# Performance work log

Hardware: AMD Instinct MI355X
Metric: run time of the kernel (lower is better)

The kernel has to match this reference:

```python
import jax, jax.numpy as jnp
import numpy as np

K_SIZE = 12      # patch kernel/stride (non-overlapping)
H, W_IMG = 60, 108
PH, PW = H // K_SIZE, W_IMG // K_SIZE
L = PH * PW
N_LAYERS = 133
EPS = 1e-12


def _unfold(x):
    # x: [B, C, 60, 108] -> [B, C*12*12, 45], matching torch.nn.Unfold ordering
    B, C = x.shape[0], x.shape[1]
    x = x.reshape(B, C, PH, K_SIZE, PW, K_SIZE)          # (b,c,ph,ki,pw,kj)
    x = x.transpose(0, 1, 3, 5, 2, 4)                    # (b,c,ki,kj,ph,pw)
    return x.reshape(B, C * K_SIZE * K_SIZE, L)


def _fold(y, C=3):
    # y: [B, C*144, 45] -> [B, C, 60, 108] (non-overlapping, so fold = inverse reshape)
    B = y.shape[0]
    y = y.reshape(B, C, K_SIZE, K_SIZE, PH, PW)          # (b,c,ki,kj,ph,pw)
    y = y.transpose(0, 1, 4, 2, 5, 3)                    # (b,c,ph,ki,pw,kj)
    return y.reshape(B, C, H, W_IMG)


def setup_inputs() -> dict:
    key = jax.random.key(0)
    k1, k2, k3 = jax.random.split(key, 3)
    I = jax.random.normal(k1, (4, 3, H, W_IMG), dtype=jnp.float32)
    S = jax.random.uniform(k2, (4, H, W_IMG, N_LAYERS), dtype=jnp.float32)
    M = jax.random.uniform(k3, (4, 1, H, W_IMG), dtype=jnp.float32)
    return {"I": I, "S": S, "M": M}


def reference(I, S, M):
    bt = I.shape[0]
    Iu = I[..., None]                  # [bt,3,60,108,1]
    Se = S[:, None]                    # [bt,1,60,108,N]
    Me = M[..., None]                  # [bt,1,60,108,1]
    U = Iu * Se * Me                   # [bt,3,60,108,N]
    Kt = Iu * Se * (1.0 - Me)
    # permute(0,4,1,2,3).reshape(bt*N, 3, 60, 108)
    U = U.transpose(0, 4, 1, 2, 3).reshape(bt * N_LAYERS, 3, H, W_IMG)
    Kt = Kt.transpose(0, 4, 1, 2, 3).reshape(bt * N_LAYERS, 3, H, W_IMG)
    Ku = _unfold(Kt)                   # [B, 432, 45]
    Uu = _unfold(U)                    # [B, 432, 45]
    # affinity: bmm(U^T, K) -> [B, 45, 45]
    Wm = jnp.einsum('bcp,bcq->bpq', Uu, Ku)
    # F.normalize(p=1, dim=-1): divide by max(L1 norm, eps)
    l1 = jnp.maximum(jnp.sum(jnp.abs(Wm), axis=-1, keepdims=True), EPS)
    Wm = Wm / l1
    # weighted sum: WK[b,c,i] = sum_j W[b,i,j] * K[b,c,j]  (same math as the
    # original broadcast multiply+sum, expressed as a batched matmul)
    WK = jnp.einsum('bij,bcj->bci', Wm, Ku)              # [B, 432, 45]
    out = _fold(WK)                                       # [B, 3, 60, 108]
    out = out.reshape(bt, N_LAYERS, 3, H, W_IMG).sum(axis=1)
    return I * (1.0 - M) + out * M
```

## Files before the change

### kernel.cpp

```cpp
#include <hip/hip_runtime.h>

#define NL 133
#define HT 60
#define WD 108
#define PIX (HT*WD)
#define CT 432
#define L45 45
#define STR 440
#define BTC 4
#define NB (BTC*NL)
#define EPIX (3*PIX)

typedef _Float16 f16;
typedef _Float16 h4v __attribute__((ext_vector_type(4)));
typedef _Float16 h8v __attribute__((ext_vector_type(8)));
typedef float f32x4 __attribute__((ext_vector_type(4)));

__device__ __forceinline__ f32x4 mfma_k32(h8v a, h8v b, f32x4 c){
  return __builtin_amdgcn_mfma_f32_16x16x32_f16(a, b, c, 0, 0, 0);
}
__device__ __forceinline__ f32x4 mfma_k16(h4v a, h4v b, f32x4 c){
  return __builtin_amdgcn_mfma_f32_16x16x16f16(a, b, c, 0, 0, 0);
}

__global__ __launch_bounds__(256) void ktrans(const float* __restrict__ S,
                                              f16* __restrict__ St){
  __shared__ float tile[64][135];
  int blk = blockIdx.x;
  int bt = blk / 102, t = blk % 102;
  int pix0 = t * 64;
  int tid = threadIdx.x;
  for (int r = tid; r < 64*NL; r += 256){
    int p = r / NL, nn = r % NL;
    int pix = pix0 + p;
    if (pix < PIX) tile[p][nn] = S[((size_t)bt*PIX + pix)*NL + nn];
  }
  __syncthreads();
  for (int w = tid; w < 64*NL; w += 256){
    int nn = w / 64, p = w % 64;
    int pix = pix0 + p;
    if (pix < PIX) St[((size_t)(bt*NL + nn))*PIX + pix] = (f16)tile[p][nn];
  }
}

template<bool USE_SCR, bool USE_ST>
__global__ __launch_bounds__(256) void kmain(const float* __restrict__ I,
                                             const float* __restrict__ S,
                                             const float* __restrict__ M,
                                             const f16* __restrict__ St,
                                             f16* __restrict__ scr,
                                             float* __restrict__ outAcc){
  __shared__ f16 lds[(L45 + 48)*STR];
  f16* bufU = lds;
  f16* bufK = lds + L45*STR;

  int b  = blockIdx.x;
  int bt = b / NL, n = b % NL;
  int tid = threadIdx.x;
  const float* Ib = I + (size_t)bt*EPIX;
  const float* Mb = M + (size_t)bt*PIX;

  for (int z = tid; z < 3*STR; z += 256) bufK[L45*STR + z] = (f16)0.f;

  for (int c = tid; c < CT; c += 256){
    int ch = c / 144, kr = c % 144;
    int ky = kr / 12, kx = kr % 12;
    const float* Ich = Ib + ch*PIX;
    int p = 0;
    #pragma unroll
    for (int py = 0; py < 5; ++py){
      int row = (py*12 + ky)*WD;
      #pragma unroll
      for (int px = 0; px < 9; ++px, ++p){
        int x = px*12 + kx;
        float sv;
        if (USE_ST) sv = (float)St[(size_t)b*PIX + row + x];
        else        sv = S[((size_t)bt*PIX + row + x)*NL + n];
        float iv = Ich[row + x];
        float mv = Mb[row + x];
        float v = iv * sv;
        float u = v * mv;
        bufU[p*STR + c] = (f16)u;
        bufK[p*STR + c] = (f16)(v - u);
      }
    }
  }
  __syncthreads();

  int wid  = tid >> 6;
  int lane = tid & 63;
  int lrow = lane & 15, lgrp = lane >> 4;

  f32x4 acc0 = {0.f,0.f,0.f,0.f}, acc1 = acc0, acc2 = acc0;
  int t0 = wid;
  int t1 = wid + 4;
  int t2 = (wid + 8 < 9) ? wid + 8 : 8;
  int ti0 = t0/3, tj0 = t0%3;
  int ti1 = t1/3, tj1 = t1%3;
  int ti2 = t2/3, tj2 = t2%3;

  const f16* uA0 = &bufU[(ti0*16 + lrow)*STR];
  const f16* uA1 = &bufU[(ti1*16 + lrow)*STR];
  const f16* uA2 = &bufU[(ti2*16 + lrow)*STR];
  const f16* kB0 = &bufK[(tj0*16 + lrow)*STR];
  const f16* kB1 = &bufK[(tj1*16 + lrow)*STR];
  const f16* kB2 = &bufK[(tj2*16 + lrow)*STR];

  for (int ks = 0; ks < 13; ++ks){
    int c0 = ks*32 + lgrp*8;
    h8v a0 = *(const h8v*)&uA0[c0];
    h8v a1 = *(const h8v*)&uA1[c0];
    h8v a2 = *(const h8v*)&uA2[c0];
    h8v b0 = *(const h8v*)&kB0[c0];
    h8v b1 = *(const h8v*)&kB1[c0];
    h8v b2 = *(const h8v*)&kB2[c0];
    acc0 = mfma_k32(a0, b0, acc0);
    acc1 = mfma_k32(a1, b1, acc1);
    acc2 = mfma_k32(a2, b2, acc2);
  }
  {
    int c0 = 416 + lgrp*4;
    h4v a0 = *(const h4v*)&uA0[c0];
    h4v a1 = *(const h4v*)&uA1[c0];
    h4v a2 = *(const h4v*)&uA2[c0];
    h4v b0 = *(const h4v*)&kB0[c0];
    h4v b1 = *(const h4v*)&kB1[c0];
    h4v b2 = *(const h4v*)&kB2[c0];
    acc0 = mfma_k16(a0, b0, acc0);
    acc1 = mfma_k16(a1, b1, acc1);
    acc2 = mfma_k16(a2, b2, acc2);
  }
  __syncthreads();

  float* Wm32 = (float*)lds;
  f16*   Wm16 = (f16*)((char*)lds + 48*49*4);
  {
    #pragma unroll
    for (int r = 0; r < 4; ++r){
      Wm32[(ti0*16 + lgrp*4 + r)*49 + tj0*16 + lrow] = acc0[r];
      Wm32[(ti1*16 + lgrp*4 + r)*49 + tj1*16 + lrow] = acc1[r];
      Wm32[(ti2*16 + lgrp*4 + r)*49 + tj2*16 + lrow] = acc2[r];
    }
  }
  __syncthreads();

  if (tid < L45){
    float rs = 0.f;
    for (int q = 0; q < L45; ++q) rs += fabsf(Wm32[tid*49 + q]);
    float inv = 1.0f / fmaxf(rs, 1e-12f);
    for (int j = 0; j < 48; ++j)
      Wm16[tid*48 + j] = (j < L45) ? (f16)(Wm32[tid*49 + j]*inv) : (f16)0.f;
  }
  __syncthreads();

  h8v aw0 = *(const h8v*)&Wm16[( 0 + lrow)*48 + lgrp*8];
  h8v aw1 = *(const h8v*)&Wm16[(16 + lrow)*48 + lgrp*8];
  h8v aw2 = *(const h8v*)&Wm16[(32 + lrow)*48 + lgrp*8];
  h4v at0 = *(const h4v*)&Wm16[( 0 + lrow)*48 + 32 + lgrp*4];
  h4v at1 = *(const h4v*)&Wm16[(16 + lrow)*48 + 32 + lgrp*4];
  h4v at2 = *(const h4v*)&Wm16[(32 + lrow)*48 + 32 + lgrp*4];

  for (int cb = wid; cb < 27; cb += 4){
    int cbase = cb*16 + lrow;
    h8v bK; h4v bT;
    #pragma unroll
    for (int r = 0; r < 8; ++r) bK[r] = bufK[(lgrp*8 + r)*STR + cbase];
    #pragma unroll
    for (int r = 0; r < 4; ++r) bT[r] = bufK[(32 + lgrp*4 + r)*STR + cbase];

    int ch  = cb / 9;
    int kr  = (cb % 9)*16 + lrow;
    int ky  = kr / 12, kx = kr - ky*12;
    int pixc = ch*PIX + ky*WD + kx;

    f32x4 d0 = {0.f,0.f,0.f,0.f}, d1 = d0, d2 = d0;
    d0 = mfma_k32(aw0, bK, d0);  d0 = mfma_k16(at0, bT, d0);
    d1 = mfma_k32(aw1, bK, d1);  d1 = mfma_k16(at1, bT, d1);
    d2 = mfma_k32(aw2, bK, d2);  d2 = mfma_k16(at2, bT, d2);

    #pragma unroll
    for (int r = 0; r < 4; ++r){
      { int i = 0 + lgrp*4 + r;
        int iy = i/9, ix = i - iy*9;
        int pix = pixc + (iy*12)*WD + ix*12;
        if (USE_SCR) scr[(size_t)b*EPIX + pix] = (f16)d0[r];
        else atomicAdd(&outAcc[(size_t)bt*EPIX + pix], (float)d0[r]); }
      { int i = 16 + lgrp*4 + r;
        int iy = i/9, ix = i - iy*9;
        int pix = pixc + (iy*12)*WD + ix*12;
        if (USE_SCR) scr[(size_t)b*EPIX + pix] = (f16)d1[r];
        else atomicAdd(&outAcc[(size_t)bt*EPIX + pix], (float)d1[r]); }
      { int i = 32 + lgrp*4 + r;
        if (i < L45){
          int iy = i/9, ix = i - iy*9;
          int pix = pixc + (iy*12)*WD + ix*12;
          if (USE_SCR) scr[(size_t)b*EPIX + pix] = (f16)d2[r];
          else atomicAdd(&outAcc[(size_t)bt*EPIX + pix], (float)d2[r]); } }
    }
  }
}

__global__ __launch_bounds__(256) void kreduce(const float* __restrict__ I,
                                               const float* __restrict__ M,
                                               const f16* __restrict__ scr,
                                               float* __restrict__ out){
  int g = blockIdx.x*256 + threadIdx.x;
  if (g >= BTC*EPIX/4) return;
  int e4 = g*4;
  int bt = e4 / EPIX, e = e4 % EPIX;
  const f16* p = scr + (size_t)bt*NL*EPIX + e;
  float a0=0.f, a1=0.f, a2=0.f, a3=0.f;
  for (int nn = 0; nn < NL; ++nn){
    h4v v = *(const h4v*)&p[(size_t)nn*EPIX];
    a0 += (float)v[0]; a1 += (float)v[1]; a2 += (float)v[2]; a3 += (float)v[3];
  }
  int pixb = e % PIX;
  const float* Mb = M + (size_t)bt*PIX;
  float4 iv = *(const float4*)&I[e4];
  float m0 = Mb[pixb], m1 = Mb[pixb+1], m2 = Mb[pixb+2], m3 = Mb[pixb+3];
  float4 o;
  o.x = iv.x*(1.f-m0) + a0*m0;
  o.y = iv.y*(1.f-m1) + a1*m1;
  o.z = iv.z*(1.f-m2) + a2*m2;
  o.w = iv.w*(1.f-m3) + a3*m3;
  *(float4*)&out[e4] = o;
}

__global__ __launch_bounds__(256) void kfinal(const float* __restrict__ I,
                                              const float* __restrict__ M,
                                              float* __restrict__ out){
  int g = blockIdx.x*256 + threadIdx.x;
  if (g >= BTC*EPIX) return;
  int bt = g / EPIX, e = g % EPIX;
  float a = out[g];
  float m = M[bt*PIX + (e % PIX)];
  out[g] = I[g]*(1.f - m) + a*m;
}

extern "C" void kernel_launch(void* const* d_in, const int* in_sizes, int n_in,
                              void* d_out, int out_size, void* d_ws, size_t ws_size,
                              hipStream_t stream){
  const float* I = (const float*)d_in[0];
  const float* S = (const float*)d_in[1];
  const float* M = (const float*)d_in[2];
  float* out = (float*)d_out;

  const size_t needScr = (size_t)NB*EPIX*sizeof(f16);
  const size_t needSt  = (size_t)NB*PIX*sizeof(f16);

  bool useScr = ws_size >= needScr;
  bool useSt;
  f16* scr = (f16*)d_ws;
  f16* St;
  if (useScr){
    useSt = ws_size >= needScr + needSt;
    St = (f16*)((char*)d_ws + needScr);
  } else {
    useSt = ws_size >= needSt;
    St = (f16*)d_ws;
  }

  if (useSt) ktrans<<<BTC*102, 256, 0, stream>>>(S, St);

  if (useScr){
    if (useSt) kmain<true ,true ><<<NB, 256, 0, stream>>>(I, S, M, St, scr, out);
    else       kmain<true ,false><<<NB, 256, 0, stream>>>(I, S, M, St, scr, out);
    kreduce<<<(BTC*EPIX/4 + 255)/256, 256, 0, stream>>>(I, M, scr, out);
  } else {
    (void)hipMemsetAsync(out, 0, (size_t)BTC*EPIX*sizeof(float), stream);
    if (useSt) kmain<false,true ><<<NB, 256, 0, stream>>>(I, S, M, St, scr, out);
    else       kmain<false,false><<<NB, 256, 0, stream>>>(I, S, M, St, scr, out);
    kfinal<<<(BTC*EPIX + 255)/256, 256, 0, stream>>>(I, M, out);
  }
}
```

Measured before the change: 117.2 us.

## Pre-unfold S and I*M into patch layout, vectorize LDS fill, split reduce

The prep kernel now writes S in the unfolded patch-major order and also precomputes the unfolded I*M and I*(1-M) tensors in fp16. The main kernel's LDS staging becomes 8-wide vector loads and fp16 multiplies, replacing scattered strided fp32 gathers. The reduce kernel splits the 133-layer sum across 8 lanes and combines them with xor shuffles to add parallelism. The products are now formed in fp16 rather than fp32 before conversion, which costs some precision, and the new workspace layout requires the prep buffers to always fit.

```diff
diff --git a/kernel.cpp b/kernel.cpp
--- a/kernel.cpp
+++ b/kernel.cpp
@@ -23,31 +23,56 @@
   return __builtin_amdgcn_mfma_f32_16x16x16f16(a, b, c, 0, 0, 0);
 }
 
-__global__ __launch_bounds__(256) void ktrans(const float* __restrict__ S,
-                                              f16* __restrict__ St){
+__global__ __launch_bounds__(256) void kprep(const float* __restrict__ S,
+                                             const float* __restrict__ I,
+                                             const float* __restrict__ M,
+                                             f16* __restrict__ Su,
+                                             f16* __restrict__ IMu,
+                                             f16* __restrict__ IKu){
   __shared__ float tile[64][135];
   int blk = blockIdx.x;
-  int bt = blk / 102, t = blk % 102;
-  int pix0 = t * 64;
   int tid = threadIdx.x;
-  for (int r = tid; r < 64*NL; r += 256){
-    int p = r / NL, nn = r % NL;
-    int pix = pix0 + p;
-    if (pix < PIX) tile[p][nn] = S[((size_t)bt*PIX + pix)*NL + nn];
-  }
-  __syncthreads();
-  for (int w = tid; w < 64*NL; w += 256){
-    int nn = w / 64, p = w % 64;
-    int pix = pix0 + p;
-    if (pix < PIX) St[((size_t)(bt*NL + nn))*PIX + pix] = (f16)tile[p][nn];
-  }
-}
-
-template<bool USE_SCR, bool USE_ST>
-__global__ __launch_bounds__(256) void kmain(const float* __restrict__ I,
-                                             const float* __restrict__ S,
-                                             const float* __restrict__ M,
-                                             const f16* __restrict__ St,
+  if (blk < BTC*102){
+    int bt = blk / 102, t = blk % 102;
+    int pix0 = t * 64;
+    for (int r = tid; r < 64*NL; r += 256){
+      int p = r / NL, nn = r % NL;
+      int pix = pix0 + p;
+      if (pix < PIX) tile[p][nn] = S[((size_t)bt*PIX + pix)*NL + nn];
+    }
+    __syncthreads();
+    for (int w = tid; w < 64*NL; w += 256){
+      int nn = w / 64, pp = w % 64;
+      int pix = pix0 + pp;
+      if (pix < PIX){
+        int y = pix / WD, x = pix % WD;
+        int py = y/12, ky = y%12, px = x/12, kx = x%12;
+        int pa = py*9 + px, kr = ky*12 + kx;
+        Su[(size_t)(bt*NL + nn)*PIX + pa*144 + kr] = (f16)tile[pp][nn];
+      }
+    }
+  } else {
+    int b2 = blk - BTC*102;
+    int bt = b2 / L45, pa = b2 % L45;
+    int py = pa/9, px = pa%9;
+    const float* Ib = I + (size_t)bt*EPIX;
+    const float* Mb = M + (size_t)bt*PIX;
+    for (int c = tid; c < CT; c += 256){
+      int ch = c/144, kr = c%144;
+      int ky = kr/12, kx = kr%12;
+      int pix = (py*12 + ky)*WD + px*12 + kx;
+      float iv = Ib[ch*PIX + pix];
+      float mv = Mb[pix];
+      IMu[((size_t)bt*L45 + pa)*CT + c] = (f16)(iv*mv);
+      IKu[((size_t)bt*L45 + pa)*CT + c] = (f16)(iv*(1.f - mv));
+    }
+  }
+}
+
+template<bool USE_SCR>
+__global__ __launch_bounds__(256) void kmain(const f16* __restrict__ IMu,
+                                             const f16* __restrict__ IKu,
+                                             const f16* __restrict__ Su,
                                              f16* __restrict__ scr,
                                              float* __restrict__ outAcc){
   __shared__ f16 lds[(L45 + 48)*STR];
@@ -55,34 +80,23 @@
   f16* bufK = lds + L45*STR;
 
   int b  = blockIdx.x;
-  int bt = b / NL, n = b % NL;
+  int bt = b / NL;
   int tid = threadIdx.x;
-  const float* Ib = I + (size_t)bt*EPIX;
-  const float* Mb = M + (size_t)bt*PIX;
 
   for (int z = tid; z < 3*STR; z += 256) bufK[L45*STR + z] = (f16)0.f;
 
-  for (int c = tid; c < CT; c += 256){
-    int ch = c / 144, kr = c % 144;
-    int ky = kr / 12, kx = kr % 12;
-    const float* Ich = Ib + ch*PIX;
-    int p = 0;
-    #pragma unroll
-    for (int py = 0; py < 5; ++py){
-      int row = (py*12 + ky)*WD;
-      #pragma unroll
-      for (int px = 0; px < 9; ++px, ++p){
-        int x = px*12 + kx;
-        float sv;
-        if (USE_ST) sv = (float)St[(size_t)b*PIX + row + x];
-        else        sv = S[((size_t)bt*PIX + row + x)*NL + n];
-        float iv = Ich[row + x];
-        float mv = Mb[row + x];
-        float v = iv * sv;
-        float u = v * mv;
-        bufU[p*STR + c] = (f16)u;
-        bufK[p*STR + c] = (f16)(v - u);
-      }
+  {
+    const f16* IMb = IMu + (size_t)bt*L45*CT;
+    const f16* IKb = IKu + (size_t)bt*L45*CT;
+    const f16* Sb  = Su  + (size_t)b*PIX;
+    for (int slot = tid; slot < L45*54; slot += 256){
+      int p = slot / 54, cg = slot % 54;
+      int c0 = cg*8;
+      h8v im = *(const h8v*)&IMb[p*CT + c0];
+      h8v ik = *(const h8v*)&IKb[p*CT + c0];
+      h8v sv = *(const h8v*)&Sb[p*144 + (c0 % 144)];
+      *(h8v*)&bufU[p*STR + c0] = im*sv;
+      *(h8v*)&bufK[p*STR + c0] = ik*sv;
     }
   }
   __syncthreads();
@@ -204,26 +218,34 @@
                                                const float* __restrict__ M,
                                                const f16* __restrict__ scr,
                                                float* __restrict__ out){
-  int g = blockIdx.x*256 + threadIdx.x;
+  int t = blockIdx.x*256 + threadIdx.x;
+  int sub = t & 7, g = t >> 3;
   if (g >= BTC*EPIX/4) return;
   int e4 = g*4;
   int bt = e4 / EPIX, e = e4 % EPIX;
   const f16* p = scr + (size_t)bt*NL*EPIX + e;
   float a0=0.f, a1=0.f, a2=0.f, a3=0.f;
-  for (int nn = 0; nn < NL; ++nn){
+  for (int nn = sub; nn < NL; nn += 8){
     h4v v = *(const h4v*)&p[(size_t)nn*EPIX];
     a0 += (float)v[0]; a1 += (float)v[1]; a2 += (float)v[2]; a3 += (float)v[3];
   }
-  int pixb = e % PIX;
-  const float* Mb = M + (size_t)bt*PIX;
-  float4 iv = *(const float4*)&I[e4];
-  float m0 = Mb[pixb], m1 = Mb[pixb+1], m2 = Mb[pixb+2], m3 = Mb[pixb+3];
-  float4 o;
-  o.x = iv.x*(1.f-m0) + a0*m0;
-  o.y = iv.y*(1.f-m1) + a1*m1;
-  o.z = iv.z*(1.f-m2) + a2*m2;
-  o.w = iv.w*(1.f-m3) + a3*m3;
-  *(float4*)&out[e4] = o;
+  #pragma unroll
+  for (int s = 1; s < 8; s <<= 1){
+    a0 += __shfl_xor(a0, s); a1 += __shfl_xor(a1, s);
+    a2 += __shfl_xor(a2, s); a3 += __shfl_xor(a3, s);
+  }
+  if (sub == 0){
+    int pixb = e % PIX;
+    const float* Mb = M + (size_t)bt*PIX;
+    float4 iv = *(const float4*)&I[e4];
+    float m0 = Mb[pixb], m1 = Mb[pixb+1], m2 = Mb[pixb+2], m3 = Mb[pixb+3];
+    float4 o;
+    o.x = iv.x*(1.f-m0) + a0*m0;
+    o.y = iv.y*(1.f-m1) + a1*m1;
+    o.z = iv.z*(1.f-m2) + a2*m2;
+    o.w = iv.w*(1.f-m3) + a3*m3;
+    *(float4*)&out[e4] = o;
+  }
 }
 
 __global__ __launch_bounds__(256) void kfinal(const float* __restrict__ I,
@@ -245,31 +267,25 @@
   const float* M = (const float*)d_in[2];
   float* out = (float*)d_out;
 
+  const size_t needSu  = (size_t)NB*PIX*sizeof(f16);
+  const size_t needIM  = (size_t)BTC*L45*CT*sizeof(f16);
   const size_t needScr = (size_t)NB*EPIX*sizeof(f16);
-  const size_t needSt  = (size_t)NB*PIX*sizeof(f16);
-
-  bool useScr = ws_size >= needScr;
-  bool useSt;
-  f16* scr = (f16*)d_ws;
-  f16* St;
+  const size_t prepSz  = needSu + 2*needIM;
+
+  f16* Su  = (f16*)d_ws;
+  f16* IMu = (f16*)((char*)d_ws + needSu);
+  f16* IKu = (f16*)((char*)d_ws + needSu + needIM);
+  f16* scr = (f16*)((char*)d_ws + prepSz);
+  bool useScr = ws_size >= prepSz + needScr;
+
+  kprep<<<BTC*102 + BTC*L45, 256, 0, stream>>>(S, I, M, Su, IMu, IKu);
+
   if (useScr){
-    useSt = ws_size >= needScr + needSt;
-    St = (f16*)((char*)d_ws + needScr);
-  } else {
-    useSt = ws_size >= needSt;
-    St = (f16*)d_ws;
-  }
-
-  if (useSt) ktrans<<<BTC*102, 256, 0, stream>>>(S, St);
-
-  if (useScr){
-    if (useSt) kmain<true ,true ><<<NB, 256, 0, stream>>>(I, S, M, St, scr, out);
-    else       kmain<true ,false><<<NB, 256, 0, stream>>>(I, S, M, St, scr, out);
-    kreduce<<<(BTC*EPIX/4 + 255)/256, 256, 0, stream>>>(I, M, scr, out);
+    kmain<true ><<<NB, 256, 0, stream>>>(IMu, IKu, Su, scr, out);
+    kreduce<<<((BTC*EPIX/4)*8 + 255)/256, 256, 0, stream>>>(I, M, scr, out);
   } else {
     (void)hipMemsetAsync(out, 0, (size_t)BTC*EPIX*sizeof(float), stream);
-    if (useSt) kmain<false,true ><<<NB, 256, 0, stream>>>(I, S, M, St, scr, out);
-    else       kmain<false,false><<<NB, 256, 0, stream>>>(I, S, M, St, scr, out);
+    kmain<false><<<NB, 256, 0, stream>>>(IMu, IKu, Su, scr, out);
     kfinal<<<(BTC*EPIX + 255)/256, 256, 0, stream>>>(I, M, out);
   }
 }
```

Result: faster. 113.8 us (-2.9%).
